# Kernel optimization log

Hardware: AMD Instinct MI355X
Metric: run time of the kernel (lower is better)

## Reference

```python
import jax, jax.numpy as jnp
import numpy as np

N_LAYERS = 12
N_CH = 256
N_IN = 4
KS = 3
SPECT_CH = 640


def conv1d(x, w, b, dilation):
    # x: [B, T, Cin], w: [K, Cin, Cout] (WIO), SAME padding, given dilation
    y = jax.lax.conv_general_dilated(
        x, w, window_strides=(1,), padding='SAME',
        rhs_dilation=(dilation,), dimension_numbers=('NWC', 'WIO', 'NWC'))
    return y + b


def setup_inputs() -> dict:
    key = jax.random.key(0)
    ks = jax.random.split(key, 16)
    s = 0.02
    inp = {}
    inp['audio'] = jax.random.normal(ks[0], (8, 4096, N_IN), dtype=jnp.float32)
    inp['spect'] = jax.random.normal(ks[1], (8, 4096, SPECT_CH), dtype=jnp.float32)
    # start 1x1 conv: [Cin, Cout]
    inp['w_start'] = jax.random.normal(ks[2], (N_IN, N_CH), dtype=jnp.float32) * s
    inp['b_start'] = jnp.zeros((N_CH,), dtype=jnp.float32)
    # dilated in_layers: stacked [L, K, Cin, 2*Cout]
    inp['w_in'] = jax.random.normal(ks[3], (N_LAYERS, KS, N_CH, 2 * N_CH), dtype=jnp.float32) * s
    inp['b_in'] = jnp.zeros((N_LAYERS, 2 * N_CH), dtype=jnp.float32)
    # cond 1x1 convs: stacked [L, SPECT_CH, 2*Cout]
    inp['w_cond'] = jax.random.normal(ks[4], (N_LAYERS, SPECT_CH, 2 * N_CH), dtype=jnp.float32) * s
    inp['b_cond'] = jnp.zeros((N_LAYERS, 2 * N_CH), dtype=jnp.float32)
    # res_skip 1x1 convs: first L-1 have 2*Cout, last has Cout
    inp['w_res'] = jax.random.normal(ks[5], (N_LAYERS - 1, N_CH, 2 * N_CH), dtype=jnp.float32) * s
    inp['b_res'] = jnp.zeros((N_LAYERS - 1, 2 * N_CH), dtype=jnp.float32)
    inp['w_res_last'] = jax.random.normal(ks[6], (N_CH, N_CH), dtype=jnp.float32) * s
    inp['b_res_last'] = jnp.zeros((N_CH,), dtype=jnp.float32)
    # end 1x1 conv (zero-initialized in the original; use small random for a
    # non-degenerate numerical baseline)
    inp['w_end'] = jax.random.normal(ks[7], (N_CH, 2 * N_IN), dtype=jnp.float32) * s
    inp['b_end'] = jnp.zeros((2 * N_IN,), dtype=jnp.float32)
    return inp


def reference(audio, spect, w_start, b_start, w_in, b_in, w_cond, b_cond,
              w_res, b_res, w_res_last, b_res_last, w_end, b_end):
    # start: 1x1 conv == matmul over channels
    started = jnp.einsum('btc,cd->btd', audio, w_start) + b_start  # [B,T,256]
    # precompute all conditioning projections: [L,B,T,512]
    cond_all = jnp.einsum('btc,lcd->lbtd', spect, w_cond) + b_cond[:, None, None, :]
    output = None
    for i in range(N_LAYERS):
        in_l = conv1d(started, w_in[i], b_in[i], 2 ** i)  # [B,T,512]
        acts = in_l + cond_all[i]
        half_tanh = jnp.tanh(acts[..., :N_CH])
        half_sig = jax.nn.sigmoid(acts[..., N_CH:])
        activated = half_tanh * half_sig  # [B,T,256]
        if i < N_LAYERS - 1:
            rs = jnp.einsum('btc,cd->btd', activated, w_res[i]) + b_res[i]
            started = started + rs[..., :N_CH]
            skip = rs[..., N_CH:]
        else:
            skip = jnp.einsum('btc,cd->btd', activated, w_res_last) + b_res_last
        output = skip if output is None else output + skip
    out = jnp.einsum('btc,cd->btd', output, w_end) + b_end  # [B,T,2*N_IN]
    return out
```

## Files before the change

kernel.cpp:

```cpp
#include <hip/hip_runtime.h>
#include <cstdint>

#define PAD 2048
#define KG 1408

typedef float f32x4 __attribute__((ext_vector_type(4)));
typedef __bf16 bf16x8 __attribute__((ext_vector_type(8)));
typedef __bf16 bf16x4 __attribute__((ext_vector_type(4)));

__device__ __forceinline__ void g2l16(const void* g, void* l) {
    __builtin_amdgcn_global_load_lds(
        (__attribute__((address_space(1))) void*)(uintptr_t)g,
        (__attribute__((address_space(3))) void*)(uint32_t)(uintptr_t)l,
        16, 0, 0);
}


__global__ void cvt_bf16_kernel(const float4* __restrict__ src, bf16x4* __restrict__ dst, int n4) {
    int idx = blockIdx.x * 256 + threadIdx.x;
    if (idx < n4) {
        float4 v = src[idx];
        bf16x4 o = {(__bf16)v.x, (__bf16)v.y, (__bf16)v.z, (__bf16)v.w};
        dst[idx] = o;
    }
}

__global__ void init_started_kernel(const float* __restrict__ audio, const float* __restrict__ w_start,
                                    const float* __restrict__ b_start, __bf16* __restrict__ started_pad) {
    int pr = blockIdx.x * 4 + (threadIdx.x >> 6);
    int c0 = (threadIdx.x & 63) * 4;
    int off = pr & 8191;
    bf16x4 o = {(__bf16)0.f, (__bf16)0.f, (__bf16)0.f, (__bf16)0.f};
    if (off >= PAD && off < PAD + 4096) {
        int r = ((pr >> 13) << 12) + (off - PAD);
        float a0 = audio[r * 4 + 0], a1 = audio[r * 4 + 1], a2 = audio[r * 4 + 2], a3 = audio[r * 4 + 3];
        for (int j = 0; j < 4; ++j) {
            int c = c0 + j;
            o[j] = (__bf16)(b_start[c] + a0 * w_start[c] + a1 * w_start[256 + c]
                            + a2 * w_start[512 + c] + a3 * w_start[768 + c]);
        }
    }
    *(bf16x4*)&started_pad[(size_t)pr * 256 + c0] = o;
}

__global__ void transpose_gate(const float* __restrict__ w_in, const float* __restrict__ w_cond,
                               __bf16* __restrict__ Wg) {
    __shared__ float tile[64][65];
    int i = blockIdx.z;
    int k0 = blockIdx.y * 64, n0 = blockIdx.x * 64;
    int tid = threadIdx.x, c = tid & 63, rr = tid >> 6;
    for (int it = 0; it < 16; ++it) {
        int kl = it * 4 + rr;
        int k = k0 + kl;
        int np = n0 + c;
        int phys = ((np >> 4) & 1) * 256 + (np >> 5) * 16 + (np & 15);
        float v;
        if (k < 768) v = w_in[((i * 3 + (k >> 8)) * 256 + (k & 255)) * 512 + phys];
        else         v = w_cond[(i * 640 + (k - 768)) * 512 + phys];
        tile[kl][c] = v;
    }
    __syncthreads();
    for (int it = 0; it < 16; ++it) {
        int nl = it * 4 + rr;
        Wg[(size_t)(i * 512 + n0 + nl) * KG + k0 + c] = (__bf16)tile[c][nl];
    }
}

__global__ void transpose_kn(const float* __restrict__ src, __bf16* __restrict__ dst,
                             int K, int N, int srcLS, int dstLS) {
    __shared__ float tile[64][65];
    int i = blockIdx.z;
    int k0 = blockIdx.y * 64, n0 = blockIdx.x * 64;
    int tid = threadIdx.x, c = tid & 63, rr = tid >> 6;
    const float* s = src + (size_t)i * srcLS;
    __bf16* dp = dst + (size_t)i * dstLS;
    for (int it = 0; it < 16; ++it) {
        int kl = it * 4 + rr;
        tile[kl][c] = s[(k0 + kl) * N + n0 + c];
    }
    __syncthreads();
    for (int it = 0; it < 16; ++it) {
        int nl = it * 4 + rr;
        dp[(size_t)(n0 + nl) * K + k0 + c] = (__bf16)tile[c][nl];
    }
}

__global__ void bias_gate_kernel(const float* __restrict__ b_in, const float* __restrict__ b_cond,
                                 float* __restrict__ bias) {
    int idx = blockIdx.x * 256 + threadIdx.x;
    int i = idx >> 9, np = idx & 511;
    int phys = ((np >> 4) & 1) * 256 + (np >> 5) * 16 + (np & 15);
    bias[idx] = b_in[i * 512 + phys] + b_cond[i * 512 + phys];
}

__global__ void wfold_kernel(const float* __restrict__ w_res, const float* __restrict__ w_res_last,
                             const float* __restrict__ w_end, const float* __restrict__ b_res,
                             const float* __restrict__ b_res_last, const float* __restrict__ b_end,
                             float* __restrict__ wfold, float* __restrict__ outconst) {
    if (blockIdx.x == 96) {
        __shared__ float red[256][8];
        int j = threadIdx.x;
        float bsum = b_res_last[j];
        for (int i = 0; i < 11; ++i) bsum += b_res[i * 512 + 256 + j];
        for (int c = 0; c < 8; ++c) red[j][c] = bsum * w_end[j * 8 + c];
        __syncthreads();
        if (j < 8) {
            float s = b_end[j];
            for (int t = 0; t < 256; ++t) s += red[t][j];
            outconst[j] = s;
        }
        return;
    }
    int idx = blockIdx.x * 256 + threadIdx.x;
    int i = idx >> 11, rem = idx & 2047, k = rem >> 3, c = rem & 7;
    float s = 0.f;
    if (i < 11) {
        const float* wr = w_res + (size_t)(i * 256 + k) * 512 + 256;
        for (int j = 0; j < 256; ++j) s += wr[j] * w_end[j * 8 + c];
    } else {
        const float* wr = w_res_last + k * 256;
        for (int j = 0; j < 256; ++j) s += wr[j] * w_end[j * 8 + c];
    }
    wfold[idx] = s;
}


__global__ __launch_bounds__(512, 2) void gate_kernel(
    const __bf16* __restrict__ started_pad, const __bf16* __restrict__ spect,
    const __bf16* __restrict__ Wg,
    const float* __restrict__ bias,
    __bf16* __restrict__ activated, int d) {
    __shared__ __align__(16) __bf16 SMEM[65536];
    const int tid = threadIdx.x;
    const int m0 = blockIdx.x * 256;
    const int n0 = blockIdx.y * 256;
    const int padbase = ((m0 >> 12) << 13) + PAD + (m0 & 4095);
    const int wave = tid >> 6, lane = tid & 63;
    const int wr = wave >> 2, wc = wave & 3;
    const int quad = lane >> 4, l15 = lane & 15;

    const int srow = tid >> 2;
    const int scw = ((tid & 3) * 8) ^ (((tid >> 3) & 3) << 3);

    f32x4 acc[8][4];
    #pragma unroll
    for (int i = 0; i < 8; i++)
        #pragma unroll
        for (int j = 0; j < 4; j++) acc[i][j] = f32x4{0.f, 0.f, 0.f, 0.f};

    auto stageA = [&](int kt, int s) {
        const __bf16* g0;
        int rs;
        if (kt < 24) {
            int tap = kt >> 3;
            int cb = (kt & 7) * 32;
            g0 = started_pad + (padbase + (tap - 1) * d) * 256 + cb + scw;
            rs = 256;
        } else {
            int cb = (kt - 24) * 32;
            g0 = spect + (size_t)m0 * 640 + cb + scw;
            rs = 640;
        }
        __bf16* As = SMEM + s * 8192;
        g2l16(g0 + srow * rs, As + tid * 8);
        g2l16(g0 + (128 + srow) * rs, As + 4096 + tid * 8);
    };
    auto stageB = [&](int kt, int s) {
        const __bf16* g0 = Wg + (size_t)(n0 + srow) * KG + kt * 32 + scw;
        __bf16* Bs = SMEM + 32768 + s * 8192;
        g2l16(g0, Bs + tid * 8);
        g2l16(g0 + 128 * KG, Bs + 4096 + tid * 8);
    };

    stageA(0, 0); stageB(0, 0);
    stageA(1, 1); stageB(1, 1);
    asm volatile("s_waitcnt vmcnt(4)" ::: "memory");
    asm volatile("s_barrier" ::: "memory");

    bf16x8 a_cur[4], b_cur[4], b_nxt[4];
    {
        const __bf16* Asl = SMEM;
        const __bf16* Bsl = SMEM + 32768;
        #pragma unroll
        for (int f = 0; f < 4; ++f) {
            int ar = wr * 128 + f * 16 + l15;
            a_cur[f] = *(const bf16x8*)&Asl[ar * 32 + ((quad * 8) ^ (((ar >> 1) & 3) << 3))];
        }
        #pragma unroll
        for (int nf = 0; nf < 4; ++nf) {
            int br = wc * 64 + nf * 16 + l15;
            b_cur[nf] = *(const bf16x8*)&Bsl[br * 32 + ((quad * 8) ^ (((br >> 1) & 3) << 3))];
        }
    }

    for (int j = 0; j < 44; ++j) {
        const int s = j & 3;
        const int sn = (j + 1) & 3;
        const __bf16* Asl = SMEM + s * 8192;

        if (j + 2 < 44) stageA(j + 2, (j + 2) & 3);
        bf16x8 a_nxt[4];
        #pragma unroll
        for (int f = 0; f < 4; ++f) {
            int ar = wr * 128 + 64 + f * 16 + l15;
            a_nxt[f] = *(const bf16x8*)&Asl[ar * 32 + ((quad * 8) ^ (((ar >> 1) & 3) << 3))];
        }
        if (j + 2 < 44) asm volatile("s_waitcnt vmcnt(2)" ::: "memory");
        else            asm volatile("s_waitcnt vmcnt(0)" ::: "memory");
        __builtin_amdgcn_s_setprio(1);
        #pragma unroll
        for (int f = 0; f < 4; ++f)
            #pragma unroll
            for (int nf = 0; nf < 4; ++nf)
                acc[f][nf] = __builtin_amdgcn_mfma_f32_16x16x32_bf16(a_cur[f], b_cur[nf], acc[f][nf], 0, 0, 0);
        __builtin_amdgcn_s_setprio(0);
        asm volatile("s_barrier" ::: "memory");

        if (j + 2 < 44) stageB(j + 2, (j + 2) & 3);
        if (j + 1 < 44) {
            const __bf16* Anl = SMEM + sn * 8192;
            const __bf16* Bnl = SMEM + 32768 + sn * 8192;
            #pragma unroll
            for (int f = 0; f < 4; ++f) {
                int ar = wr * 128 + f * 16 + l15;
                a_cur[f] = *(const bf16x8*)&Anl[ar * 32 + ((quad * 8) ^ (((ar >> 1) & 3) << 3))];
            }
            #pragma unroll
            for (int nf = 0; nf < 4; ++nf) {
                int br = wc * 64 + nf * 16 + l15;
                b_nxt[nf] = *(const bf16x8*)&Bnl[br * 32 + ((quad * 8) ^ (((br >> 1) & 3) << 3))];
            }
        }
        __builtin_amdgcn_s_setprio(1);
        #pragma unroll
        for (int f = 0; f < 4; ++f)
            #pragma unroll
            for (int nf = 0; nf < 4; ++nf)
                acc[4 + f][nf] = __builtin_amdgcn_mfma_f32_16x16x32_bf16(a_nxt[f], b_cur[nf], acc[4 + f][nf], 0, 0, 0);
        __builtin_amdgcn_s_setprio(0);
        if (j + 1 < 44) {
            #pragma unroll
            for (int nf = 0; nf < 4; ++nf) b_cur[nf] = b_nxt[nf];
        }
    }

    __syncthreads();

    __bf16* tile = SMEM;
    #pragma unroll
    for (int nj = 0; nj < 2; ++nj) {
        int colT = wc * 64 + nj * 32 + l15;
        float bt = bias[n0 + colT];
        float bs = bias[n0 + colT + 16];
        int chl = wc * 32 + nj * 16 + l15;
        #pragma unroll
        for (int mi = 0; mi < 8; ++mi) {
            #pragma unroll
            for (int reg = 0; reg < 4; ++reg) {
                int row = wr * 128 + mi * 16 + quad * 4 + reg;
                float xt = acc[mi][2 * nj][reg] + bt;
                float xs = acc[mi][2 * nj + 1][reg] + bs;
                float th = 2.f / (1.f + __expf(-2.f * xt)) - 1.f;
                float sg = 1.f / (1.f + __expf(-xs));
                tile[row * 132 + chl] = (__bf16)(th * sg);
            }
        }
    }
    __syncthreads();
    int chb = n0 >> 1;
    for (int pass = 0; pass < 8; ++pass) {
        int row = (tid >> 4) + 32 * pass;
        int seg = tid & 15;
        bf16x8 v = *(const bf16x8*)&tile[row * 132 + seg * 8];
        *(bf16x8*)&activated[(m0 + row) * 256 + chb + seg * 8] = v;
    }
}

__global__ __launch_bounds__(256) void res_kernel(
    const __bf16* __restrict__ activated, const __bf16* __restrict__ Wr,
    const float* __restrict__ b_res,
    const float* __restrict__ wfold,
    const float* __restrict__ outconst,
    __bf16* __restrict__ started_pad, float* __restrict__ out, int initOut) {
    __shared__ __align__(16) __bf16 As[128 * 32];
    __shared__ __align__(16) __bf16 Bs[128 * 32];
    __shared__ __align__(16) __bf16 WfB[16 * 264];
    const int tid = threadIdx.x;
    const int m0 = blockIdx.x * 128;
    const int n0 = blockIdx.y * 128;
    const int srow = tid >> 2;
    const int skq = (tid & 3) * 8;
    const int wave = tid >> 6, lane = tid & 63;
    const int wm = (wave >> 1) * 64, wn = (wave & 1) * 64;
    const int quad = lane >> 4, l15 = lane & 15;
    const bool doOut = (blockIdx.y == 0);
    const bool outWave = doOut && (wn == 0);

    f32x4 acc[4][4];
    for (int i = 0; i < 4; i++)
        for (int j = 0; j < 4; j++) acc[i][j] = f32x4{0.f, 0.f, 0.f, 0.f};
    f32x4 acc_o[4];
    for (int i = 0; i < 4; i++) acc_o[i] = f32x4{0.f, 0.f, 0.f, 0.f};

    const __bf16* Abase = activated + (m0 + srow) * 256 + skq;
    const __bf16* Bbase = Wr + (n0 + srow) * 256 + skq;

    if (doOut) {
        for (int t = 0; t < 16; ++t) {
            int e = t * 256 + tid;
            int col = e >> 8, k = e & 255;
            WfB[col * 264 + k] = (col < 8) ? (__bf16)wfold[k * 8 + col] : (__bf16)0.f;
        }
    }

    for (int ks = 0; ks < 8; ++ks) {
        int kk = ks * 32;
        g2l16(Abase + kk, &As[srow * 32 + skq]);
        g2l16(Abase + kk + 64 * 256, &As[(64 + srow) * 32 + skq]);
        g2l16(Bbase + kk, &Bs[srow * 32 + skq]);
        g2l16(Bbase + kk + 64 * 256, &Bs[(64 + srow) * 32 + skq]);
        __syncthreads();
        bf16x8 a[4], b[4];
        for (int mi = 0; mi < 4; mi++) a[mi] = *(const bf16x8*)&As[(wm + mi * 16 + l15) * 32 + quad * 8];
        for (int ni = 0; ni < 4; ni++) b[ni] = *(const bf16x8*)&Bs[(wn + ni * 16 + l15) * 32 + quad * 8];
        for (int mi = 0; mi < 4; mi++)
            for (int ni = 0; ni < 4; ni++)
                acc[mi][ni] = __builtin_amdgcn_mfma_f32_16x16x32_bf16(a[mi], b[ni], acc[mi][ni], 0, 0, 0);
        if (outWave) {
            bf16x8 bx = *(const bf16x8*)&WfB[l15 * 264 + kk + quad * 8];
            for (int mi = 0; mi < 4; mi++)
                acc_o[mi] = __builtin_amdgcn_mfma_f32_16x16x32_bf16(a[mi], bx, acc_o[mi], 0, 0, 0);
        }
        __syncthreads();
    }

    for (int ni = 0; ni < 4; ++ni) {
        int col = n0 + wn + ni * 16 + l15;
        float bcol = b_res[col];
        for (int mi = 0; mi < 4; ++mi) {
            for (int reg = 0; reg < 4; ++reg) {
                int r = m0 + wm + mi * 16 + quad * 4 + reg;
                int pr = ((r >> 12) << 13) + PAD + (r & 4095);
                int idx = pr * 256 + col;
                float f = (float)started_pad[idx] + acc[mi][ni][reg] + bcol;
                started_pad[idx] = (__bf16)f;
            }
        }
    }
    if (outWave && l15 < 8) {
        for (int mi = 0; mi < 4; ++mi) {
            for (int reg = 0; reg < 4; ++reg) {
                int r = m0 + wm + mi * 16 + quad * 4 + reg;
                float base = initOut ? outconst[l15] : out[r * 8 + l15];
                out[r * 8 + l15] = base + acc_o[mi][reg];
            }
        }
    }
}

__global__ __launch_bounds__(256) void outacc_kernel(
    const __bf16* __restrict__ activated, const float* __restrict__ wfold,
    float* __restrict__ out) {
    __shared__ __align__(16) float Wf[2048];
    int tid = threadIdx.x;
    ((float4*)Wf)[tid] = ((const float4*)wfold)[tid];
    ((float4*)Wf)[256 + tid] = ((const float4*)wfold)[256 + tid];
    __syncthreads();
    int row2 = tid >> 1, half = tid & 1;
    int r = blockIdx.x * 128 + row2;
    const bf16x8* ap = (const bf16x8*)(activated + r * 256);
    const float4* wf = (const float4*)Wf;
    float ox = 0.f, oy = 0.f, oz = 0.f, ow = 0.f;
    for (int c8 = 0; c8 < 32; ++c8) {
        bf16x8 av = ap[c8];
        for (int e = 0; e < 8; ++e) {
            float a = (float)av[e];
            float4 w = wf[(c8 * 8 + e) * 2 + half];
            ox += a * w.x; oy += a * w.y; oz += a * w.z; ow += a * w.w;
        }
    }
    float4* op = (float4*)&out[r * 8 + half * 4];
    float4 o = *op;
    o.x += ox; o.y += oy; o.z += oz; o.w += ow;
    *op = o;
}


extern "C" void kernel_launch(void* const* d_in, const int* in_sizes, int n_in,
                              void* d_out, int out_size, void* d_ws, size_t ws_size,
                              hipStream_t stream) {
    const float* audio      = (const float*)d_in[0];
    const float* spect      = (const float*)d_in[1];
    const float* w_start    = (const float*)d_in[2];
    const float* b_start    = (const float*)d_in[3];
    const float* w_in       = (const float*)d_in[4];
    const float* b_in       = (const float*)d_in[5];
    const float* w_cond     = (const float*)d_in[6];
    const float* b_cond     = (const float*)d_in[7];
    const float* w_res      = (const float*)d_in[8];
    const float* b_res      = (const float*)d_in[9];
    const float* w_res_last = (const float*)d_in[10];
    const float* b_res_last = (const float*)d_in[11];
    const float* w_end      = (const float*)d_in[12];
    const float* b_end      = (const float*)d_in[13];
    float* out = (float*)d_out;

    char* ws = (char*)d_ws;
    __bf16* started_pad = (__bf16*)ws; ws += 33554432;
    __bf16* activated   = (__bf16*)ws; ws += 16777216;
    __bf16* spect_bf    = (__bf16*)ws; ws += 41943040;
    __bf16* Wg          = (__bf16*)ws; ws += 17301504;
    __bf16* Wr          = (__bf16*)ws; ws += 1441792;
    float*  wfold       = (float*)ws;  ws += 98304;
    float*  biasg       = (float*)ws;  ws += 24576;
    float*  outconst    = (float*)ws;  ws += 256;

    init_started_kernel<<<dim3(16384), 256, 0, stream>>>(audio, w_start, b_start, started_pad);
    cvt_bf16_kernel<<<dim3(20480), 256, 0, stream>>>((const float4*)spect, (bf16x4*)spect_bf, 5242880);
    transpose_gate<<<dim3(8, 22, 12), 256, 0, stream>>>(w_in, w_cond, Wg);
    transpose_kn<<<dim3(4, 4, 11), 256, 0, stream>>>(w_res, Wr, 256, 512, 256 * 512, 256 * 256);
    bias_gate_kernel<<<dim3(24), 256, 0, stream>>>(b_in, b_cond, biasg);
    wfold_kernel<<<dim3(97), 256, 0, stream>>>(w_res, w_res_last, w_end, b_res, b_res_last, b_end,
                                               wfold, outconst);

    for (int i = 0; i < 12; ++i) {
        gate_kernel<<<dim3(128, 2), 512, 0, stream>>>(
            started_pad, spect_bf, Wg + (size_t)i * 512 * KG, biasg + i * 512, activated, 1 << i);
        if (i < 11) {
            res_kernel<<<dim3(256, 2), 256, 0, stream>>>(
                activated, Wr + (size_t)i * 256 * 256, b_res + i * 512,
                wfold + i * 2048, outconst, started_pad, out, i == 0 ? 1 : 0);
        } else {
            outacc_kernel<<<dim3(256), 256, 0, stream>>>(activated, wfold + 11 * 2048, out);
        }
    }
}
```

Measured before the change: 1.036 ms.

## Restructure gate GEMM mainloop to 64-wide K tiles with double buffering

Changes the gate kernel's main loop from 44 K-steps of 32 with a 4-stage ring buffer to 22 K-steps of 64 with 2-stage double buffering. It uses a new 8-way XOR swizzle and splits each step into four MFMA quadrants, with global-to-LDS prefetch of the next tile interleaved between quadrants. The goal is fewer loop iterations and barriers per K element, and more MFMA work per LDS fetch. In exchange it adds more barriers within each step, waits for all outstanding loads at the end of every step, and keeps larger fragments in registers, which may hurt overlap.

```diff
diff --git a/kernel.cpp b/kernel.cpp
--- a/kernel.cpp
+++ b/kernel.cpp
@@ -139,8 +139,8 @@
     const int wr = wave >> 2, wc = wave & 3;
     const int quad = lane >> 4, l15 = lane & 15;
 
-    const int srow = tid >> 2;
-    const int scw = ((tid & 3) * 8) ^ (((tid >> 3) & 3) << 3);
+    const int co0 = (quad ^ (l15 & 7)) * 8;
+    const int co1 = co0 ^ 32;
 
     f32x4 acc[8][4];
     #pragma unroll
@@ -148,103 +148,124 @@
         #pragma unroll
         for (int j = 0; j < 4; j++) acc[i][j] = f32x4{0.f, 0.f, 0.f, 0.f};
 
-    auto stageA = [&](int kt, int s) {
-        const __bf16* g0;
-        int rs;
-        if (kt < 24) {
-            int tap = kt >> 3;
-            int cb = (kt & 7) * 32;
-            g0 = started_pad + (padbase + (tap - 1) * d) * 256 + cb + scw;
-            rs = 256;
+    const int srr = tid >> 3;
+    const int sswz = (((tid & 7) ^ (srr & 7)) * 8);
+
+    auto stageA = [&](int T, int h) {
+        __bf16* dst = SMEM + (T & 1) * 16384 + h * 8192 + tid * 8;
+        if (T < 12) {
+            const int tap = T >> 2;
+            const int cb = (T & 3) * 64;
+            const __bf16* g = started_pad + (size_t)(padbase + h * 128 + (tap - 1) * d) * 256 + cb + sswz;
+            g2l16(g + srr * 256, dst);
+            g2l16(g + (64 + srr) * 256, dst + 4096);
         } else {
-            int cb = (kt - 24) * 32;
-            g0 = spect + (size_t)m0 * 640 + cb + scw;
-            rs = 640;
-        }
-        __bf16* As = SMEM + s * 8192;
-        g2l16(g0 + srow * rs, As + tid * 8);
-        g2l16(g0 + (128 + srow) * rs, As + 4096 + tid * 8);
+            const int cb = (T - 12) * 64;
+            const __bf16* g = spect + (size_t)(m0 + h * 128) * 640 + cb + sswz;
+            g2l16(g + srr * 640, dst);
+            g2l16(g + (64 + srr) * 640, dst + 4096);
+        }
     };
-    auto stageB = [&](int kt, int s) {
-        const __bf16* g0 = Wg + (size_t)(n0 + srow) * KG + kt * 32 + scw;
-        __bf16* Bs = SMEM + 32768 + s * 8192;
-        g2l16(g0, Bs + tid * 8);
-        g2l16(g0 + 128 * KG, Bs + 4096 + tid * 8);
+    auto stageB = [&](int T, int h) {
+        const __bf16* g = Wg + (size_t)(n0 + h * 128) * KG + T * 64 + sswz;
+        __bf16* dst = SMEM + 32768 + (T & 1) * 16384 + h * 8192 + tid * 8;
+        g2l16(g + srr * KG, dst);
+        g2l16(g + (64 + srr) * KG, dst + 4096);
     };
 
-    stageA(0, 0); stageB(0, 0);
-    stageA(1, 1); stageB(1, 1);
-    asm volatile("s_waitcnt vmcnt(4)" ::: "memory");
+    stageA(0, 0); stageA(0, 1); stageB(0, 0); stageB(0, 1);
+    asm volatile("s_waitcnt vmcnt(0)" ::: "memory");
     asm volatile("s_barrier" ::: "memory");
 
-    bf16x8 a_cur[4], b_cur[4], b_nxt[4];
-    {
-        const __bf16* Asl = SMEM;
-        const __bf16* Bsl = SMEM + 32768;
+    bf16x8 a[4][2], bl[2][2], bh[2][2];
+
+    for (int T = 0; T < 22; ++T) {
+        const __bf16* As = SMEM + (T & 1) * 16384;
+        const __bf16* Bs = SMEM + 32768 + (T & 1) * 16384;
+        const bool pf = (T + 1 < 22);
+
         #pragma unroll
         for (int f = 0; f < 4; ++f) {
             int ar = wr * 128 + f * 16 + l15;
-            a_cur[f] = *(const bf16x8*)&Asl[ar * 32 + ((quad * 8) ^ (((ar >> 1) & 3) << 3))];
-        }
-        #pragma unroll
-        for (int nf = 0; nf < 4; ++nf) {
-            int br = wc * 64 + nf * 16 + l15;
-            b_cur[nf] = *(const bf16x8*)&Bsl[br * 32 + ((quad * 8) ^ (((br >> 1) & 3) << 3))];
-        }
-    }
-
-    for (int j = 0; j < 44; ++j) {
-        const int s = j & 3;
-        const int sn = (j + 1) & 3;
-        const __bf16* Asl = SMEM + s * 8192;
-
-        if (j + 2 < 44) stageA(j + 2, (j + 2) & 3);
-        bf16x8 a_nxt[4];
+            a[f][0] = *(const bf16x8*)&As[ar * 64 + co0];
+            a[f][1] = *(const bf16x8*)&As[ar * 64 + co1];
+        }
+        #pragma unroll
+        for (int g = 0; g < 2; ++g) {
+            int br = wc * 64 + g * 16 + l15;
+            bl[g][0] = *(const bf16x8*)&Bs[br * 64 + co0];
+            bl[g][1] = *(const bf16x8*)&Bs[br * 64 + co1];
+        }
+        if (pf) { stageA(T + 1, 0); stageA(T + 1, 1); }
+        asm volatile("s_barrier" ::: "memory");
+        asm volatile("s_waitcnt lgkmcnt(0)" ::: "memory");
+        __builtin_amdgcn_sched_barrier(0);
+        __builtin_amdgcn_s_setprio(1);
+        #pragma unroll
+        for (int f = 0; f < 4; ++f)
+            #pragma unroll
+            for (int g = 0; g < 2; ++g) {
+                acc[f][g] = __builtin_amdgcn_mfma_f32_16x16x32_bf16(a[f][0], bl[g][0], acc[f][g], 0, 0, 0);
+                acc[f][g] = __builtin_amdgcn_mfma_f32_16x16x32_bf16(a[f][1], bl[g][1], acc[f][g], 0, 0, 0);
+            }
+        __builtin_amdgcn_s_setprio(0);
+        asm volatile("s_barrier" ::: "memory");
+
+        #pragma unroll
+        for (int g = 0; g < 2; ++g) {
+            int br = wc * 64 + 32 + g * 16 + l15;
+            bh[g][0] = *(const bf16x8*)&Bs[br * 64 + co0];
+            bh[g][1] = *(const bf16x8*)&Bs[br * 64 + co1];
+        }
+        if (pf) stageB(T + 1, 0);
+        asm volatile("s_barrier" ::: "memory");
+        asm volatile("s_waitcnt lgkmcnt(0)" ::: "memory");
+        __builtin_amdgcn_sched_barrier(0);
+        __builtin_amdgcn_s_setprio(1);
+        #pragma unroll
+        for (int f = 0; f < 4; ++f)
+            #pragma unroll
+            for (int g = 0; g < 2; ++g) {
+                acc[f][2 + g] = __builtin_amdgcn_mfma_f32_16x16x32_bf16(a[f][0], bh[g][0], acc[f][2 + g], 0, 0, 0);
+                acc[f][2 + g] = __builtin_amdgcn_mfma_f32_16x16x32_bf16(a[f][1], bh[g][1], acc[f][2 + g], 0, 0, 0);
+            }
+        __builtin_amdgcn_s_setprio(0);
+        asm volatile("s_barrier" ::: "memory");
+
         #pragma unroll
         for (int f = 0; f < 4; ++f) {
             int ar = wr * 128 + 64 + f * 16 + l15;
-            a_nxt[f] = *(const bf16x8*)&Asl[ar * 32 + ((quad * 8) ^ (((ar >> 1) & 3) << 3))];
-        }
-        if (j + 2 < 44) asm volatile("s_waitcnt vmcnt(2)" ::: "memory");
-        else            asm volatile("s_waitcnt vmcnt(0)" ::: "memory");
+            a[f][0] = *(const bf16x8*)&As[ar * 64 + co0];
+            a[f][1] = *(const bf16x8*)&As[ar * 64 + co1];
+        }
+        if (pf) stageB(T + 1, 1);
+        asm volatile("s_barrier" ::: "memory");
+        asm volatile("s_waitcnt lgkmcnt(0)" ::: "memory");
+        __builtin_amdgcn_sched_barrier(0);
         __builtin_amdgcn_s_setprio(1);
         #pragma unroll
         for (int f = 0; f < 4; ++f)
             #pragma unroll
-            for (int nf = 0; nf < 4; ++nf)
-                acc[f][nf] = __builtin_amdgcn_mfma_f32_16x16x32_bf16(a_cur[f], b_cur[nf], acc[f][nf], 0, 0, 0);
+            for (int g = 0; g < 2; ++g) {
+                acc[4 + f][g] = __builtin_amdgcn_mfma_f32_16x16x32_bf16(a[f][0], bl[g][0], acc[4 + f][g], 0, 0, 0);
+                acc[4 + f][g] = __builtin_amdgcn_mfma_f32_16x16x32_bf16(a[f][1], bl[g][1], acc[4 + f][g], 0, 0, 0);
+            }
         __builtin_amdgcn_s_setprio(0);
         asm volatile("s_barrier" ::: "memory");
 
-        if (j + 2 < 44) stageB(j + 2, (j + 2) & 3);
-        if (j + 1 < 44) {
-            const __bf16* Anl = SMEM + sn * 8192;
-            const __bf16* Bnl = SMEM + 32768 + sn * 8192;
-            #pragma unroll
-            for (int f = 0; f < 4; ++f) {
-                int ar = wr * 128 + f * 16 + l15;
-                a_cur[f] = *(const bf16x8*)&Anl[ar * 32 + ((quad * 8) ^ (((ar >> 1) & 3) << 3))];
-            }
-            #pragma unroll
-            for (int nf = 0; nf < 4; ++nf) {
-                int br = wc * 64 + nf * 16 + l15;
-                b_nxt[nf] = *(const bf16x8*)&Bnl[br * 32 + ((quad * 8) ^ (((br >> 1) & 3) << 3))];
-            }
-        }
+        asm volatile("s_barrier" ::: "memory");
         __builtin_amdgcn_s_setprio(1);
         #pragma unroll
         for (int f = 0; f < 4; ++f)
             #pragma unroll
-            for (int nf = 0; nf < 4; ++nf)
-                acc[4 + f][nf] = __builtin_amdgcn_mfma_f32_16x16x32_bf16(a_nxt[f], b_cur[nf], acc[4 + f][nf], 0, 0, 0);
+            for (int g = 0; g < 2; ++g) {
+                acc[4 + f][2 + g] = __builtin_amdgcn_mfma_f32_16x16x32_bf16(a[f][0], bh[g][0], acc[4 + f][2 + g], 0, 0, 0);
+                acc[4 + f][2 + g] = __builtin_amdgcn_mfma_f32_16x16x32_bf16(a[f][1], bh[g][1], acc[4 + f][2 + g], 0, 0, 0);
+            }
         __builtin_amdgcn_s_setprio(0);
-        if (j + 1 < 44) {
-            #pragma unroll
-            for (int nf = 0; nf < 4; ++nf) b_cur[nf] = b_nxt[nf];
-        }
-    }
-
-    __syncthreads();
+        asm volatile("s_waitcnt vmcnt(0)" ::: "memory");
+        asm volatile("s_barrier" ::: "memory");
+    }
 
     __bf16* tile = SMEM;
     #pragma unroll
```

New measurement: 1.041 ms. Within noise of the previous version (+0.5%).

## Double-buffer res_kernel LDS loads, swizzle layout, and vectorize residual epilogue

Applied to the files above, without the earlier changes.

The residual GEMM kernel now double-buffers its A/B LDS tiles, issuing the next k-step's global-to-LDS loads before computing the current one, so only one barrier per step is needed. An XOR swizzle on the LDS column layout is meant to reduce bank conflicts on the MFMA operand reads. The epilogue stages accumulators through a shared float tile and then does coalesced 16-byte read-modify-writes of started_pad instead of scattered scalar bf16 accesses. These changes add LDS usage (double buffers plus a 64x132 float tile), which may reduce occupancy.

```diff
diff --git a/kernel.cpp b/kernel.cpp
--- a/kernel.cpp
+++ b/kernel.cpp
@@ -282,14 +282,16 @@
     const float* __restrict__ wfold,
     const float* __restrict__ outconst,
     __bf16* __restrict__ started_pad, float* __restrict__ out, int initOut) {
-    __shared__ __align__(16) __bf16 As[128 * 32];
-    __shared__ __align__(16) __bf16 Bs[128 * 32];
+    __shared__ __align__(16) __bf16 As[2][128 * 32];
+    __shared__ __align__(16) __bf16 Bs[2][128 * 32];
     __shared__ __align__(16) __bf16 WfB[16 * 264];
+    __shared__ __align__(16) float Tile[64 * 132];
     const int tid = threadIdx.x;
     const int m0 = blockIdx.x * 128;
     const int n0 = blockIdx.y * 128;
+    const int padbase = ((m0 >> 12) << 13) + PAD + (m0 & 4095);
     const int srow = tid >> 2;
-    const int skq = (tid & 3) * 8;
+    const int swcol = ((tid & 3) ^ ((srow >> 1) & 3)) * 8;
     const int wave = tid >> 6, lane = tid & 63;
     const int wm = (wave >> 1) * 64, wn = (wave & 1) * 64;
     const int quad = lane >> 4, l15 = lane & 15;
@@ -302,8 +304,16 @@
     f32x4 acc_o[4];
     for (int i = 0; i < 4; i++) acc_o[i] = f32x4{0.f, 0.f, 0.f, 0.f};
 
-    const __bf16* Abase = activated + (m0 + srow) * 256 + skq;
-    const __bf16* Bbase = Wr + (n0 + srow) * 256 + skq;
+    const __bf16* Abase = activated + (m0 + srow) * 256 + swcol;
+    const __bf16* Bbase = Wr + (n0 + srow) * 256 + swcol;
+
+    auto stage = [&](int ks, int s) {
+        int kk = ks * 32;
+        g2l16(Abase + kk, &As[s][tid * 8]);
+        g2l16(Abase + kk + 64 * 256, &As[s][tid * 8 + 2048]);
+        g2l16(Bbase + kk, &Bs[s][tid * 8]);
+        g2l16(Bbase + kk + 64 * 256, &Bs[s][tid * 8 + 2048]);
+    };
 
     if (doOut) {
         for (int t = 0; t < 16; ++t) {
@@ -313,40 +323,58 @@
         }
     }
 
+    stage(0, 0);
+    __syncthreads();
+
     for (int ks = 0; ks < 8; ++ks) {
-        int kk = ks * 32;
-        g2l16(Abase + kk, &As[srow * 32 + skq]);
-        g2l16(Abase + kk + 64 * 256, &As[(64 + srow) * 32 + skq]);
-        g2l16(Bbase + kk, &Bs[srow * 32 + skq]);
-        g2l16(Bbase + kk + 64 * 256, &Bs[(64 + srow) * 32 + skq]);
-        __syncthreads();
+        const int cur = ks & 1;
+        if (ks + 1 < 8) stage(ks + 1, cur ^ 1);
         bf16x8 a[4], b[4];
-        for (int mi = 0; mi < 4; mi++) a[mi] = *(const bf16x8*)&As[(wm + mi * 16 + l15) * 32 + quad * 8];
-        for (int ni = 0; ni < 4; ni++) b[ni] = *(const bf16x8*)&Bs[(wn + ni * 16 + l15) * 32 + quad * 8];
+        for (int mi = 0; mi < 4; mi++) {
+            int row = wm + mi * 16 + l15;
+            a[mi] = *(const bf16x8*)&As[cur][row * 32 + ((quad ^ ((row >> 1) & 3)) * 8)];
+        }
+        for (int ni = 0; ni < 4; ni++) {
+            int row = wn + ni * 16 + l15;
+            b[ni] = *(const bf16x8*)&Bs[cur][row * 32 + ((quad ^ ((row >> 1) & 3)) * 8)];
+        }
         for (int mi = 0; mi < 4; mi++)
             for (int ni = 0; ni < 4; ni++)
                 acc[mi][ni] = __builtin_amdgcn_mfma_f32_16x16x32_bf16(a[mi], b[ni], acc[mi][ni], 0, 0, 0);
         if (outWave) {
-            bf16x8 bx = *(const bf16x8*)&WfB[l15 * 264 + kk + quad * 8];
+            bf16x8 bx = *(const bf16x8*)&WfB[l15 * 264 + ks * 32 + quad * 8];
             for (int mi = 0; mi < 4; mi++)
                 acc_o[mi] = __builtin_amdgcn_mfma_f32_16x16x32_bf16(a[mi], bx, acc_o[mi], 0, 0, 0);
         }
         __syncthreads();
     }
 
-    for (int ni = 0; ni < 4; ++ni) {
-        int col = n0 + wn + ni * 16 + l15;
-        float bcol = b_res[col];
-        for (int mi = 0; mi < 4; ++mi) {
-            for (int reg = 0; reg < 4; ++reg) {
-                int r = m0 + wm + mi * 16 + quad * 4 + reg;
-                int pr = ((r >> 12) << 13) + PAD + (r & 4095);
-                int idx = pr * 256 + col;
-                float f = (float)started_pad[idx] + acc[mi][ni][reg] + bcol;
-                started_pad[idx] = (__bf16)f;
+    for (int half = 0; half < 2; ++half) {
+        if ((wm >> 6) == half) {
+            for (int ni = 0; ni < 4; ++ni) {
+                int colL = wn + ni * 16 + l15;
+                float bcol = b_res[n0 + colL];
+                for (int mi = 0; mi < 4; ++mi)
+                    for (int reg = 0; reg < 4; ++reg)
+                        Tile[(mi * 16 + quad * 4 + reg) * 132 + colL] = acc[mi][ni][reg] + bcol;
             }
         }
-    }
+        __syncthreads();
+        int row = tid >> 2;
+        int cs = (tid & 3) * 32;
+        __bf16* sp = started_pad + (size_t)(padbase + half * 64 + row) * 256 + n0 + cs;
+        const float* tp = Tile + row * 132 + cs;
+        #pragma unroll
+        for (int v = 0; v < 4; ++v) {
+            bf16x8 curv = *(const bf16x8*)&sp[v * 8];
+            bf16x8 o;
+            #pragma unroll
+            for (int e = 0; e < 8; ++e) o[e] = (__bf16)((float)curv[e] + tp[v * 8 + e]);
+            *(bf16x8*)&sp[v * 8] = o;
+        }
+        __syncthreads();
+    }
+
     if (outWave && l15 < 8) {
         for (int mi = 0; mi < 4; ++mi) {
             for (int reg = 0; reg < 4; ++reg) {
```

Result: slower. 1.074 ms (+3.7%).
